# Kernel optimization log

Hardware: AMD Instinct MI355X
Metric: run time of the kernel (lower is better)

The kernel has to match this reference:

```python
import jax, jax.numpy as jnp
import numpy as np


def _conv1x1_relu(x, w, b):
    # x: [b,c,h,w], w: [o,c], b: [o]
    y = jnp.einsum('bchw,oc->bohw', x, w) + b[None, :, None, None]
    return jax.nn.relu(y)


def setup_inputs() -> dict:
    key = jax.random.key(0)
    k1, k2, k3, k4, k5 = jax.random.split(key, 5)
    C, CI = 256, 32  # in_channels, inter_channels (reduction=8)
    features = jax.random.normal(k1, (4, C, 64, 64), dtype=jnp.float32)
    w_red = jax.random.normal(k2, (CI, C), dtype=jnp.float32) * 0.05
    b_red = jax.random.normal(k3, (CI,), dtype=jnp.float32) * 0.05
    w_val = jax.random.normal(k4, (C, C), dtype=jnp.float32) * 0.05
    b_val = jax.random.normal(k5, (C,), dtype=jnp.float32) * 0.05
    return {"features": features, "w_red": w_red, "b_red": b_red,
            "w_val": w_val, "b_val": b_val}


def reference(features, w_red, b_red, w_val, b_val):
    b, C, h, w = features.shape
    ins = _conv1x1_relu(features, w_red, b_red)          # [b,ci,h,w]
    ci = ins.shape[1]
    A = ins.transpose(0, 2, 3, 1).reshape(b, h * w, ci)  # [b,hw,ci]
    # pairwise squared L2 distance, then exp(-D)
    A2 = jnp.einsum('bnc,bmc->bnm', A, A)                # [b,hw,hw]
    sq = jnp.sum(A * A, axis=-1)                         # [b,hw]
    D = sq[:, :, None] + sq[:, None, :] - 2.0 * A2
    similarity_mask = jax.nn.sigmoid(jnp.exp(-D))        # [b,hw,hw]
    val = _conv1x1_relu(features, w_val, b_val)          # [b,C,h,w]
    val_flat = val.reshape(b, C, h * w)
    weight_mask = jnp.einsum('bcn,bnm->bcm', val_flat, similarity_mask)
    out = weight_mask.reshape(b, C, h, w) + features
    return (out, similarity_mask)
```

## Files before the change

kernel.cpp:

```cpp
#include <hip/hip_runtime.h>
#include <cstdint>
#include <cstddef>

typedef __attribute__((ext_vector_type(8))) short short8;
typedef __attribute__((ext_vector_type(4))) float f32x4;

#define MFMA16(a,b,c) __builtin_amdgcn_mfma_f32_16x16x32_bf16((a),(b),(c),0,0,0)

static __device__ __forceinline__ unsigned short f2bf(float f) {
  union { float f; unsigned u; } v; v.f = f;
  unsigned r = v.u + 0x7fffu + ((v.u >> 16) & 1u);
  return (unsigned short)(r >> 16);
}
static __device__ __forceinline__ float bf2f(unsigned short h) {
  union { unsigned u; float f; } v; v.u = ((unsigned)h) << 16;
  return v.f;
}

__global__ __launch_bounds__(256) void k_wcvt(const float* __restrict__ w_val,
                                              const float* __restrict__ w_red,
                                              unsigned short* __restrict__ wv,
                                              unsigned short* __restrict__ wr) {
  int i = blockIdx.x * 256 + threadIdx.x;
  if (i < 65536) wv[i] = f2bf(w_val[i]);
  int j = i - 65536;
  if (j >= 0 && j < 8192) wr[j] = f2bf(w_red[j]);
}

__global__ __launch_bounds__(512) void k_prep(const float* __restrict__ feat,
                                              const unsigned short* __restrict__ wv,
                                              const unsigned short* __restrict__ wr,
                                              const float* __restrict__ b_red,
                                              const float* __restrict__ b_val,
                                              unsigned short* __restrict__ A,
                                              float* __restrict__ sq,
                                              unsigned short* __restrict__ val) {
  __shared__ unsigned short smT[32][264];
  __shared__ float sqp[2][32];
  const int t = threadIdx.x, w = t >> 6, lane = t & 63, a = lane & 15, g = lane >> 4;
  const int b = blockIdx.y, p0 = blockIdx.x * 32;
  const float* fb = feat + (size_t)b * 256 * 4096;
  {
    const int p = t & 31, cg = t >> 5;
#pragma unroll
    for (int it = 0; it < 4; ++it) {
      int c0 = cg * 4 + it * 64;
      const float* src = fb + (size_t)c0 * 4096 + p0 + p;
      unsigned short u0 = f2bf(src[0]);
      unsigned short u1 = f2bf(src[4096]);
      unsigned short u2 = f2bf(src[8192]);
      unsigned short u3 = f2bf(src[12288]);
      uint2 pk;
      pk.x = u0 | ((unsigned)u1 << 16);
      pk.y = u2 | ((unsigned)u3 << 16);
      *(uint2*)&smT[p][c0] = pk;
    }
  }
  __syncthreads();

  f32x4 accv[2][2] = {};
  const int rs = w & 1, rms = (w >> 1) & 1;
  f32x4 accr = {0, 0, 0, 0};
#pragma unroll
  for (int kk = 0; kk < 8; ++kk) {
    short8 bfr[2];
#pragma unroll
    for (int ms = 0; ms < 2; ++ms)
      bfr[ms] = *(const short8*)&smT[ms * 16 + a][kk * 32 + g * 8];
#pragma unroll
    for (int s = 0; s < 2; ++s) {
      short8 af = *(const short8*)&wv[(w * 32 + s * 16 + a) * 256 + kk * 32 + g * 8];
#pragma unroll
      for (int ms = 0; ms < 2; ++ms)
        accv[s][ms] = MFMA16(af, bfr[ms], accv[s][ms]);
    }
    if (w < 4) {
      short8 wrf = *(const short8*)&wr[(rs * 16 + a) * 256 + kk * 32 + g * 8];
      accr = MFMA16(bfr[rms], wrf, accr);
    }
  }
#pragma unroll
  for (int s = 0; s < 2; ++s) {
    f32x4 bv = *(const f32x4*)&b_val[w * 32 + s * 16 + g * 4];
#pragma unroll
    for (int ms = 0; ms < 2; ++ms) {
#pragma unroll
      for (int r = 0; r < 4; ++r) {
        float v = accv[s][ms][r] + bv[r];
        v = v > 0.f ? v : 0.f;
        int o = w * 32 + s * 16 + g * 4 + r;
        val[((size_t)(b * 256 + o)) * 4096 + p0 + ms * 16 + a] = f2bf(v);
      }
    }
  }
  if (w < 4) {
    float bias = b_red[rs * 16 + a];
    float rsum[4];
    unsigned short* Ab = A + ((size_t)b * 4096 + p0 + rms * 16) * 32;
#pragma unroll
    for (int r = 0; r < 4; ++r) {
      float v = accr[r] + bias;
      v = v > 0.f ? v : 0.f;
      unsigned short h = f2bf(v);
      Ab[(g * 4 + r) * 32 + rs * 16 + a] = h;
      float vb = bf2f(h);
      rsum[r] = vb * vb;
    }
#pragma unroll
    for (int off = 1; off < 16; off <<= 1) {
#pragma unroll
      for (int r = 0; r < 4; ++r) rsum[r] += __shfl_xor(rsum[r], off, 64);
    }
    if (a == 0) {
#pragma unroll
      for (int r = 0; r < 4; ++r) sqp[rs][rms * 16 + g * 4 + r] = rsum[r];
    }
  }
  __syncthreads();
  if (t < 32) sq[(size_t)b * 4096 + p0 + t] = sqp[0][t] + sqp[1][t];
}

__global__ __launch_bounds__(1024) void k_fused(const unsigned short* __restrict__ A,
                                                const float* __restrict__ sq,
                                                const unsigned short* __restrict__ val,
                                                const float* __restrict__ feat,
                                                float* __restrict__ dout) {
  __shared__ unsigned short ldsT[2][64][72];
  __shared__ float ldsF[2][64][68];
  const int t = threadIdx.x, w = t >> 6, lane = t & 63, a = lane & 15, g = lane >> 4;
  const int nsub = w & 3, msub = w >> 2;
  const int lin = blockIdx.x + (blockIdx.y << 6);
  const int swz = (lin & 7) * 32 + (lin >> 3);
  const int b = swz >> 6, m0 = (swz & 63) * 64;
  const unsigned short* Ab = A + (size_t)b * 4096 * 32;
  const float* sqb = sq + (size_t)b * 4096;
  const unsigned short* vb = val + ((size_t)b * 256 + w * 16) * 4096;
  float* maskout = dout + 4194304 + (size_t)b * 16777216;

  const int mrow = m0 + msub * 16 + a;
  const short8 am = *(const short8*)&Ab[(size_t)mrow * 32 + g * 8];
  const float sqm = sqb[mrow];
  f32x4 acc[4] = {};
  const f32x4 zero = {0, 0, 0, 0};

  short8 vf_c[2], vf_n[2];

  {
    short8 an0 = *(const short8*)&Ab[(size_t)(nsub * 16 + a) * 32 + g * 8];
    f32x4 sqn0 = *(const f32x4*)&sqb[nsub * 16 + g * 4];
    f32x4 sfr = MFMA16(an0, am, zero);
    f32x4 mkv;
#pragma unroll
    for (int r = 0; r < 4; ++r) {
      float u = __expf(fmaf(2.f, sfr[r], -(sqn0[r] + sqm)));
      float u2 = u * u;
      float pa = fmaf(u2, 2.0833333e-3f, -2.0833333e-2f);
      float pb = fmaf(u2, pa, 0.25f);
      mkv[r] = fmaf(u, pb, 0.5f);
    }
    uint2 pk;
    pk.x = f2bf(mkv[0]) | ((unsigned)f2bf(mkv[1]) << 16);
    pk.y = f2bf(mkv[2]) | ((unsigned)f2bf(mkv[3]) << 16);
    *(uint2*)&ldsT[0][msub * 16 + a][nsub * 16 + g * 4] = pk;
    *(f32x4*)&ldsF[0][msub * 16 + a][nsub * 16 + g * 4] = mkv;
  }
  vf_c[0] = *(const short8*)&vb[(size_t)a * 4096 + g * 8];
  vf_c[1] = *(const short8*)&vb[(size_t)a * 4096 + 32 + g * 8];
  asm volatile("s_waitcnt lgkmcnt(0)\n\ts_barrier" ::: "memory");

#pragma unroll 2
  for (int tt = 0; tt < 64; ++tt) {
    const int n0 = tt * 64, n1 = n0 + 64, buf = tt & 1;
    short8 an_n;
    f32x4 sqn_n;
    if (tt < 63) {
      an_n = *(const short8*)&Ab[(size_t)(n1 + nsub * 16 + a) * 32 + g * 8];
      sqn_n = *(const f32x4*)&sqb[n1 + nsub * 16 + g * 4];
      vf_n[0] = *(const short8*)&vb[(size_t)a * 4096 + n1 + g * 8];
      vf_n[1] = *(const short8*)&vb[(size_t)a * 4096 + n1 + 32 + g * 8];
    }
#pragma unroll
    for (int ks = 0; ks < 2; ++ks) {
      short8 bfr[4];
#pragma unroll
      for (int ms = 0; ms < 4; ++ms)
        bfr[ms] = *(const short8*)&ldsT[buf][ms * 16 + a][ks * 32 + g * 8];
#pragma unroll
      for (int ms = 0; ms < 4; ++ms)
        acc[ms] = MFMA16(vf_c[ks], bfr[ms], acc[ms]);
    }
#pragma unroll
    for (int j = 0; j < 4; ++j) {
      float mv = ldsF[buf][w * 4 + j][lane];
      __builtin_nontemporal_store(mv, &maskout[(size_t)(m0 + w * 4 + j) * 4096 + n0 + lane]);
    }
    if (tt < 63) {
      f32x4 sfr = MFMA16(an_n, am, zero);
      f32x4 mkv;
#pragma unroll
      for (int r = 0; r < 4; ++r) {
        float u = __expf(fmaf(2.f, sfr[r], -(sqn_n[r] + sqm)));
        float u2 = u * u;
        float pa = fmaf(u2, 2.0833333e-3f, -2.0833333e-2f);
        float pb = fmaf(u2, pa, 0.25f);
        mkv[r] = fmaf(u, pb, 0.5f);
      }
      uint2 pk;
      pk.x = f2bf(mkv[0]) | ((unsigned)f2bf(mkv[1]) << 16);
      pk.y = f2bf(mkv[2]) | ((unsigned)f2bf(mkv[3]) << 16);
      *(uint2*)&ldsT[buf ^ 1][msub * 16 + a][nsub * 16 + g * 4] = pk;
      *(f32x4*)&ldsF[buf ^ 1][msub * 16 + a][nsub * 16 + g * 4] = mkv;
    }
    asm volatile("s_waitcnt lgkmcnt(0)\n\ts_barrier" ::: "memory");
    vf_c[0] = vf_n[0];
    vf_c[1] = vf_n[1];
  }
  const float* fb = feat + (size_t)b * 256 * 4096;
  float* ob = dout + (size_t)b * 256 * 4096;
#pragma unroll
  for (int ms = 0; ms < 4; ++ms) {
#pragma unroll
    for (int r = 0; r < 4; ++r) {
      int c = w * 16 + g * 4 + r;
      int m = m0 + ms * 16 + a;
      size_t idx = (size_t)c * 4096 + m;
      float fv = __builtin_nontemporal_load(&fb[idx]);
      __builtin_nontemporal_store(acc[ms][r] + fv, &ob[idx]);
    }
  }
}

extern "C" void kernel_launch(void* const* d_in, const int* in_sizes, int n_in,
                              void* d_out, int out_size, void* d_ws, size_t ws_size,
                              hipStream_t stream) {
  const float* feat  = (const float*)d_in[0];
  const float* w_red = (const float*)d_in[1];
  const float* b_red = (const float*)d_in[2];
  const float* w_val = (const float*)d_in[3];
  const float* b_val = (const float*)d_in[4];
  float* out = (float*)d_out;
  char* ws = (char*)d_ws;
  unsigned short* A   = (unsigned short*)ws;
  float*          sq  = (float*)        (ws + 1048576);
  unsigned short* wv  = (unsigned short*)(ws + 1114112);
  unsigned short* wr  = (unsigned short*)(ws + 1245184);
  unsigned short* val = (unsigned short*)(ws + 1261568);

  k_wcvt<<<dim3(288), 256, 0, stream>>>(w_val, w_red, wv, wr);
  k_prep<<<dim3(128, 4), 512, 0, stream>>>(feat, wv, wr, b_red, b_val, A, sq, val);
  k_fused<<<dim3(64, 4), 1024, 0, stream>>>(A, sq, val, feat, out);
}
```

Measured before the change: 142.6 us.

## Retile value GEMM into 2x2 warp tiles and store mask directly from registers

The float mask staging buffer in shared memory is removed, and each wave now writes its 16x16 mask fragment straight to global memory as 16-byte nontemporal stores. The value-times-mask GEMM is retiled so each wave covers 32 channels by 32 positions (a 2x2 MFMA tile) instead of 16 channels by 64 positions. This halves the LDS reads of mask fragments per wave but doubles the global loads of value fragments. The aim is to cut LDS traffic and footprint and drop the LDS-to-global copy. The trade-off is less coalesced mask writes, since each lane writes 16 bytes in a row-strided pattern, plus more value load bandwidth.

```diff
diff --git a/kernel.cpp b/kernel.cpp
--- a/kernel.cpp
+++ b/kernel.cpp
@@ -126,24 +126,24 @@
                                                 const float* __restrict__ feat,
                                                 float* __restrict__ dout) {
   __shared__ unsigned short ldsT[2][64][72];
-  __shared__ float ldsF[2][64][68];
   const int t = threadIdx.x, w = t >> 6, lane = t & 63, a = lane & 15, g = lane >> 4;
   const int nsub = w & 3, msub = w >> 2;
+  const int cg = w & 7, mg = w >> 3;
   const int lin = blockIdx.x + (blockIdx.y << 6);
   const int swz = (lin & 7) * 32 + (lin >> 3);
   const int b = swz >> 6, m0 = (swz & 63) * 64;
   const unsigned short* Ab = A + (size_t)b * 4096 * 32;
   const float* sqb = sq + (size_t)b * 4096;
-  const unsigned short* vb = val + ((size_t)b * 256 + w * 16) * 4096;
+  const unsigned short* vb = val + ((size_t)b * 256 + cg * 32) * 4096;
   float* maskout = dout + 4194304 + (size_t)b * 16777216;
 
   const int mrow = m0 + msub * 16 + a;
   const short8 am = *(const short8*)&Ab[(size_t)mrow * 32 + g * 8];
   const float sqm = sqb[mrow];
-  f32x4 acc[4] = {};
+  f32x4 acc[2][2] = {};
   const f32x4 zero = {0, 0, 0, 0};
 
-  short8 vf_c[2], vf_n[2];
+  short8 vf_c[2][2], vf_n[2][2];
 
   {
     short8 an0 = *(const short8*)&Ab[(size_t)(nsub * 16 + a) * 32 + g * 8];
@@ -162,10 +162,13 @@
     pk.x = f2bf(mkv[0]) | ((unsigned)f2bf(mkv[1]) << 16);
     pk.y = f2bf(mkv[2]) | ((unsigned)f2bf(mkv[3]) << 16);
     *(uint2*)&ldsT[0][msub * 16 + a][nsub * 16 + g * 4] = pk;
-    *(f32x4*)&ldsF[0][msub * 16 + a][nsub * 16 + g * 4] = mkv;
-  }
-  vf_c[0] = *(const short8*)&vb[(size_t)a * 4096 + g * 8];
-  vf_c[1] = *(const short8*)&vb[(size_t)a * 4096 + 32 + g * 8];
+    __builtin_nontemporal_store(mkv, (f32x4*)&maskout[(size_t)mrow * 4096 + nsub * 16 + g * 4]);
+  }
+#pragma unroll
+  for (int cs = 0; cs < 2; ++cs)
+#pragma unroll
+    for (int ks = 0; ks < 2; ++ks)
+      vf_c[cs][ks] = *(const short8*)&vb[(size_t)(cs * 16 + a) * 4096 + ks * 32 + g * 8];
   asm volatile("s_waitcnt lgkmcnt(0)\n\ts_barrier" ::: "memory");
 
 #pragma unroll 2
@@ -176,23 +179,23 @@
     if (tt < 63) {
       an_n = *(const short8*)&Ab[(size_t)(n1 + nsub * 16 + a) * 32 + g * 8];
       sqn_n = *(const f32x4*)&sqb[n1 + nsub * 16 + g * 4];
-      vf_n[0] = *(const short8*)&vb[(size_t)a * 4096 + n1 + g * 8];
-      vf_n[1] = *(const short8*)&vb[(size_t)a * 4096 + n1 + 32 + g * 8];
+#pragma unroll
+      for (int cs = 0; cs < 2; ++cs)
+#pragma unroll
+        for (int ks = 0; ks < 2; ++ks)
+          vf_n[cs][ks] = *(const short8*)&vb[(size_t)(cs * 16 + a) * 4096 + n1 + ks * 32 + g * 8];
     }
 #pragma unroll
     for (int ks = 0; ks < 2; ++ks) {
-      short8 bfr[4];
-#pragma unroll
-      for (int ms = 0; ms < 4; ++ms)
-        bfr[ms] = *(const short8*)&ldsT[buf][ms * 16 + a][ks * 32 + g * 8];
-#pragma unroll
-      for (int ms = 0; ms < 4; ++ms)
-        acc[ms] = MFMA16(vf_c[ks], bfr[ms], acc[ms]);
-    }
-#pragma unroll
-    for (int j = 0; j < 4; ++j) {
-      float mv = ldsF[buf][w * 4 + j][lane];
-      __builtin_nontemporal_store(mv, &maskout[(size_t)(m0 + w * 4 + j) * 4096 + n0 + lane]);
+      short8 bfr[2];
+#pragma unroll
+      for (int ms = 0; ms < 2; ++ms)
+        bfr[ms] = *(const short8*)&ldsT[buf][mg * 32 + ms * 16 + a][ks * 32 + g * 8];
+#pragma unroll
+      for (int cs = 0; cs < 2; ++cs)
+#pragma unroll
+        for (int ms = 0; ms < 2; ++ms)
+          acc[cs][ms] = MFMA16(vf_c[cs][ks], bfr[ms], acc[cs][ms]);
     }
     if (tt < 63) {
       f32x4 sfr = MFMA16(an_n, am, zero);
@@ -209,23 +212,28 @@
       pk.x = f2bf(mkv[0]) | ((unsigned)f2bf(mkv[1]) << 16);
       pk.y = f2bf(mkv[2]) | ((unsigned)f2bf(mkv[3]) << 16);
       *(uint2*)&ldsT[buf ^ 1][msub * 16 + a][nsub * 16 + g * 4] = pk;
-      *(f32x4*)&ldsF[buf ^ 1][msub * 16 + a][nsub * 16 + g * 4] = mkv;
+      __builtin_nontemporal_store(mkv, (f32x4*)&maskout[(size_t)mrow * 4096 + n1 + nsub * 16 + g * 4]);
     }
     asm volatile("s_waitcnt lgkmcnt(0)\n\ts_barrier" ::: "memory");
-    vf_c[0] = vf_n[0];
-    vf_c[1] = vf_n[1];
+#pragma unroll
+    for (int cs = 0; cs < 2; ++cs)
+#pragma unroll
+      for (int ks = 0; ks < 2; ++ks) vf_c[cs][ks] = vf_n[cs][ks];
   }
   const float* fb = feat + (size_t)b * 256 * 4096;
   float* ob = dout + (size_t)b * 256 * 4096;
 #pragma unroll
-  for (int ms = 0; ms < 4; ++ms) {
-#pragma unroll
-    for (int r = 0; r < 4; ++r) {
-      int c = w * 16 + g * 4 + r;
-      int m = m0 + ms * 16 + a;
-      size_t idx = (size_t)c * 4096 + m;
-      float fv = __builtin_nontemporal_load(&fb[idx]);
-      __builtin_nontemporal_store(acc[ms][r] + fv, &ob[idx]);
+  for (int cs = 0; cs < 2; ++cs) {
+#pragma unroll
+    for (int ms = 0; ms < 2; ++ms) {
+#pragma unroll
+      for (int r = 0; r < 4; ++r) {
+        int c = cg * 32 + cs * 16 + g * 4 + r;
+        int m = m0 + mg * 32 + ms * 16 + a;
+        size_t idx = (size_t)c * 4096 + m;
+        float fv = __builtin_nontemporal_load(&fb[idx]);
+        __builtin_nontemporal_store(acc[cs][ms][r] + fv, &ob[idx]);
+      }
     }
   }
 }
```

After: 184.3 us. 29.3% more time.
